# Kernel tuning notes

Measured on AMD Instinct MI355X. Metric: run time of the kernel, lower is better.

## Reference

```python
import jax, jax.numpy as jnp
import numpy as np

ENERGY = 0.4  # target low-frequency energy ratio (ctor default energy=0.4)


def setup_inputs() -> dict:
    key = jax.random.key(0)
    x = jax.random.normal(key, (8, 64, 256, 256), dtype=jnp.float32)
    return {"x": x}


def _min_cutoff_map(H, W):
    """For each pixel of the fftshifted spectrum, the smallest cutoff c such that
    the pixel lies inside the central box [crow-c:crow+c, ccol-c:ccol+c].
    A pixel (r, cc) is inside iff c >= max(-dr, dr+1) and c >= max(-dc, dc+1)."""
    crow, ccol = H // 2, W // 2
    dr = np.arange(H) - crow
    dc = np.arange(W) - ccol
    mr = np.maximum(-dr, dr + 1)
    mc = np.maximum(-dc, dc + 1)
    return np.maximum(mr[:, None], mc[None, :]).astype(np.int32)  # [H, W]


def reference(x):
    B, C, H, W = x.shape
    # fp32 FFT (matches the autocast-disabled fft in the original)
    fshift = jnp.fft.fftshift(jnp.fft.fft2(x.astype(jnp.float32)), axes=(-2, -1))

    minc = jnp.asarray(_min_cutoff_map(H, W))          # [H, W] int32
    nseg = max(H // 2, W // 2) + 1                      # static
    K = min(H, W) // 2                                  # candidates are 1..K-1

    # Radial (box) cumulative energy profile of channel 0, one pass per sample.
    mag2 = jnp.abs(fshift[:, 0]) ** 2                   # [B, H, W]
    ids = minc.reshape(-1)
    per_box = jax.vmap(
        lambda m: jax.ops.segment_sum(m.reshape(-1), ids, num_segments=nseg)
    )(mag2)                                             # [B, nseg]
    cum = jnp.cumsum(per_box, axis=-1)                  # cum[b, c] = box-energy at cutoff c
    total = cum[:, -1]
    target = ENERGY * total

    found = cum[:, 1:K] >= target[:, None]              # candidates c = 1..K-1
    first = jnp.argmax(found, axis=-1) + 1              # smallest satisfying c
    cutoff = jnp.where(jnp.any(found, axis=-1), first, 5)  # fallback 5, as in torch

    # Zero the central box per sample (broadcast over channels), then inverse FFT.
    keep = (minc[None, None, :, :] > cutoff[:, None, None, None]).astype(jnp.float32)
    hp = fshift * keep
    out = jnp.abs(jnp.fft.ifft2(jnp.fft.ifftshift(hp, axes=(-2, -1))))
    return out
```

## Files before the change

### kernel.cpp

```cpp
#include <hip/hip_runtime.h>
#include <hip/hip_fp16.h>
#include <math.h>

#define RESERVE 16384

__device__ __forceinline__ float2 cadd(float2 a, float2 b){ return make_float2(a.x+b.x, a.y+b.y); }
__device__ __forceinline__ float2 csub(float2 a, float2 b){ return make_float2(a.x-b.x, a.y-b.y); }
__device__ __forceinline__ float2 cmul(float2 a, float2 b){ return make_float2(a.x*b.x - a.y*b.y, a.x*b.y + a.y*b.x); }
__device__ __forceinline__ float2 cmulc(float2 a, float2 b){
  return make_float2(a.x*b.x + a.y*b.y, a.x*b.y - a.y*b.x); }
__device__ __forceinline__ __half2 f2h(float2 v){ return __floats2half2_rn(v.x, v.y); }
__device__ __forceinline__ float2 h2f(__half2 h){ return __half22float2(h); }

#define SCHED_FENCE() __builtin_amdgcn_sched_barrier(0x7F)

__device__ __forceinline__ constexpr int rho4(int r) { return ((r & 3) << 2) | (r >> 2); }

template<int DIR> __device__ __forceinline__ float2 twc(float2 z, float c, float s) {
  const float si = (DIR < 0) ? s : -s;
  return make_float2(c*z.x - si*z.y, c*z.y + si*z.x);
}
template<int DIR> __device__ __forceinline__ float2 mulmi(float2 z) {
  return (DIR < 0) ? make_float2(z.y, -z.x) : make_float2(-z.y, z.x);
}

template<int DIR, bool REV>
__device__ __forceinline__ void fft16(float2* v) {
  #define IX(i) (REV ? rho4(i) : (i))
  #pragma unroll
  for (int j0 = 0; j0 < 4; ++j0) {
    float2 a0 = v[IX(j0)], a1 = v[IX(j0+4)], a2 = v[IX(j0+8)], a3 = v[IX(j0+12)];
    float2 t0 = cadd(a0,a2), t1 = csub(a0,a2), t2 = cadd(a1,a3), d = csub(a1,a3);
    float2 t3 = (DIR < 0) ? make_float2(d.y,-d.x) : make_float2(-d.y,d.x);
    v[IX(j0)]    = cadd(t0,t2);
    v[IX(j0+4)]  = cadd(t1,t3);
    v[IX(j0+8)]  = csub(t0,t2);
    v[IX(j0+12)] = csub(t1,t3);
  }
  v[IX(5)]  = twc<DIR>(v[IX(5)],  0.92387953f, -0.38268343f);
  v[IX(6)]  = twc<DIR>(v[IX(6)],  0.70710678f, -0.70710678f);
  v[IX(7)]  = twc<DIR>(v[IX(7)],  0.38268343f, -0.92387953f);
  v[IX(9)]  = twc<DIR>(v[IX(9)],  0.70710678f, -0.70710678f);
  v[IX(10)] = mulmi<DIR>(v[IX(10)]);
  v[IX(11)] = twc<DIR>(v[IX(11)], -0.70710678f, -0.70710678f);
  v[IX(13)] = twc<DIR>(v[IX(13)],  0.38268343f, -0.92387953f);
  v[IX(14)] = twc<DIR>(v[IX(14)], -0.70710678f, -0.70710678f);
  v[IX(15)] = twc<DIR>(v[IX(15)], -0.92387953f,  0.38268343f);
  #pragma unroll
  for (int k1 = 0; k1 < 4; ++k1) {
    float2 a0 = v[IX(4*k1)], a1 = v[IX(4*k1+1)], a2 = v[IX(4*k1+2)], a3 = v[IX(4*k1+3)];
    float2 t0 = cadd(a0,a2), t1 = csub(a0,a2), t2 = cadd(a1,a3), d = csub(a1,a3);
    float2 t3 = (DIR < 0) ? make_float2(d.y,-d.x) : make_float2(-d.y,d.x);
    v[IX(4*k1)]   = cadd(t0,t2);
    v[IX(4*k1+1)] = cadd(t1,t3);
    v[IX(4*k1+2)] = csub(t0,t2);
    v[IX(4*k1+3)] = csub(t1,t3);
  }
  #undef IX
}

__device__ __forceinline__ void make_twf(int l, float2* twf) {
  float s, c;
  sincospif((float)l * (-1.0f/128.0f), &s, &c);
  const float2 w = make_float2(c, s);
  twf[0] = make_float2(1.f, 0.f);
  #pragma unroll
  for (int k = 1; k < 16; ++k) twf[k] = cmul(twf[k-1], w);
}

template<int DIR, bool REV1, bool HB>
__device__ __forceinline__ void fft256g(float2* v, void* trb, int l, const float2* twf) {
  fft16<DIR, REV1>(v);
  #pragma unroll
  for (int r = 0; r < 16; ++r) {
    const int k1 = REV1 ? r : rho4(r);
    float2 z = v[r];
    z = (DIR < 0) ? cmul(twf[k1], z) : cmulc(twf[k1], z);
    const int idx = (k1 << 4) | (l ^ k1);
    if (HB) ((__half2*)trb)[idx] = f2h(z);
    else    ((float2*)trb)[idx] = z;
  }
  SCHED_FENCE();
  #pragma unroll
  for (int j = 0; j < 16; ++j) {
    const int idx = (l << 4) | (j ^ l);
    v[j] = HB ? h2f(((__half2*)trb)[idx]) : ((float2*)trb)[idx];
  }
  SCHED_FENCE();
  fft16<DIR, false>(v);
}

__global__ __launch_bounds__(256) void k_pass1(const float* __restrict__ x,
    __half2* __restrict__ Bt, int img0, int istep) {
  __shared__ __align__(16) char smraw[16 * 264 * 8];
  float2*  trb  = (float2*)smraw;
  __half2* tile = (__half2*)smraw;
  const int tid = threadIdx.x, g = tid >> 4, l = tid & 15;
  const int slot = blockIdx.y, img = img0 + slot * istep;
  float2 twf[16]; make_twf(l, twf);
  const float* xim = x + ((size_t)img << 16);
  __half2* bim = Bt + ((size_t)slot << 16);
  float2* tb = trb + g * 264;
  #pragma unroll 1
  for (int it = 0; it < 4; ++it) {
    const int row = (blockIdx.x << 6) + (it << 4) + g;
    const float* xr = xim + (row << 8);
    float2 v[16];
    #pragma unroll
    for (int j = 0; j < 16; ++j) v[j] = make_float2(xr[l + (j << 4)], 0.f);
    fft256g<-1, false, false>(v, tb, l, twf);
    __syncthreads();
    #pragma unroll
    for (int rr = 0; rr < 16; ++rr)
      tile[(l + (rho4(rr) << 4)) * 17 + g] = f2h(v[rr]);
    __syncthreads();
    const int rbase = (blockIdx.x << 6) + (it << 4);
    const int rloc = tid & 15, ub = tid >> 4;
    #pragma unroll
    for (int jj = 0; jj < 16; ++jj) {
      const int u = (jj << 4) + ub;
      bim[(u << 8) + rbase + rloc] = tile[u * 17 + rloc];
    }
    __syncthreads();
  }
}

__global__ __launch_bounds__(256) void k_pass2(const __half2* __restrict__ Bt,
    __half2* __restrict__ Ct, const int* __restrict__ cutoffs, int img0, int istep) {
  __shared__ __align__(16) char smraw[256 * 17 * 4];
  __half2* trb  = (__half2*)smraw;
  __half2* tile = (__half2*)smraw;
  const int tid = threadIdx.x, g = tid >> 4, l = tid & 15;
  const int slot = blockIdx.y, img = img0 + slot * istep;
  const int cut = cutoffs[img >> 6];
  float2 twf[16]; make_twf(l, twf);
  const __half2* bim = Bt + ((size_t)slot << 16);
  __half2* cim = Ct + ((size_t)slot << 16);
  __half2* tb = trb + g * 264;
  #pragma unroll 1
  for (int it = 0; it < 4; ++it) {
    const int u = (blockIdx.x << 6) + (it << 4) + g;
    const __half2* col = bim + (u << 8);
    float2 v[16];
    #pragma unroll
    for (int j = 0; j < 16; ++j) v[j] = h2f(col[l + (j << 4)]);
    fft256g<-1, false, true>(v, tb, l, twf);
    if ((u < cut) | (u >= 256 - cut)) {
      #pragma unroll
      for (int rr = 0; rr < 16; ++rr) {
        const int vi = l + (rho4(rr) << 4);
        if (vi < cut || vi >= 256 - cut) v[rr] = make_float2(0.f, 0.f);
      }
    }
    fft256g<1, true, true>(v, tb, l, twf);
    __syncthreads();
    #pragma unroll
    for (int rr = 0; rr < 16; ++rr)
      tile[(l + (rho4(rr) << 4)) * 17 + g] = f2h(v[rr]);
    __syncthreads();
    const int ubase = (blockIdx.x << 6) + (it << 4);
    const int cloc = tid & 15, rb = tid >> 4;
    #pragma unroll
    for (int jj = 0; jj < 16; ++jj) {
      const int r = (jj << 4) + rb;
      cim[(r << 8) + ubase + cloc] = tile[r * 17 + cloc];
    }
    __syncthreads();
  }
}

__global__ __launch_bounds__(256) void k_pass3(const __half2* __restrict__ Ct,
    float* __restrict__ out, int img0, int istep) {
  __shared__ __half2 trbs[16 * 264];
  const int tid = threadIdx.x, g = tid >> 4, l = tid & 15;
  const int slot = blockIdx.y, img = img0 + slot * istep;
  float2 twf[16]; make_twf(l, twf);
  #pragma unroll
  for (int k = 0; k < 16; ++k) { twf[k].x *= 0.0625f; twf[k].y *= 0.0625f; }
  const __half2* cim = Ct + ((size_t)slot << 16);
  float* oim = out + ((size_t)img << 16);
  __half2* tb = trbs + g * 264;
  #pragma unroll 1
  for (int it = 0; it < 4; ++it) {
    const int row = (blockIdx.x << 6) + (it << 4) + g;
    const __half2* rp = cim + (row << 8);
    float2 v[16];
    #pragma unroll
    for (int j = 0; j < 16; ++j) v[j] = h2f(rp[l + (j << 4)]);
    fft256g<1, false, true>(v, tb, l, twf);
    float* orow = oim + (row << 8);
    #pragma unroll
    for (int rr = 0; rr < 16; ++rr) {
      const float2 z = v[rr];
      orow[l + (rho4(rr) << 4)] = sqrtf(z.x*z.x + z.y*z.y) * (1.f/4096.f);
    }
  }
}

__global__ __launch_bounds__(256) void k_hist(const __half2* __restrict__ Bt,
    double* __restrict__ bins, int slot0, int sstep, int batch0) {
  __shared__ float2 trbuf[16 * 256];
  __shared__ float whist[4][132];
  const int tid = threadIdx.x, g = tid >> 4, l = tid & 15, wave = tid >> 6;
  const int lb = blockIdx.y;
  const int batch = batch0 + lb;
  const size_t slot = (size_t)(slot0 + lb * sstep);
  const int u = (blockIdx.x << 4) + g;
  float2 twf[16]; make_twf(l, twf);
  for (int i = tid & 63; i < 132; i += 64) whist[wave][i] = 0.f;
  __syncthreads();
  const __half2* col = Bt + (slot << 16) + (u << 8);
  float2 v[16];
  #pragma unroll
  for (int j = 0; j < 16; ++j) v[j] = h2f(col[l + (j << 4)]);
  float2* tb = trbuf + (g << 8);
  fft256g<-1, false, false>(v, tb, l, twf);
  const int fc = (u < 128) ? u + 1 : 256 - u;
  #pragma unroll
  for (int rr = 0; rr < 16; ++rr) {
    const int vi = l + (rho4(rr) << 4);
    const int fu = (vi < 128) ? vi + 1 : 256 - vi;
    const int seg = fu > fc ? fu : fc;
    const float2 z = v[rr];
    atomicAdd(&whist[wave][seg], z.x*z.x + z.y*z.y);
  }
  __syncthreads();
  for (int s = tid; s < 129; s += 256) {
    const float sum = whist[0][s] + whist[1][s] + whist[2][s] + whist[3][s];
    if (sum != 0.f) atomicAdd(&bins[batch * 129 + s], (double)sum);
  }
}

__global__ void k_cutoff(const double* __restrict__ bins, int* __restrict__ cutoffs) {
  const int b = threadIdx.x;
  if (b < 8) {
    const double* Bv = bins + b * 129;
    double total = 0.0;
    for (int s = 0; s < 129; ++s) total += Bv[s];
    const double target = 0.4 * total;
    double cum = Bv[0];
    int cut = 5;
    bool found = false;
    for (int s = 1; s <= 127; ++s) {
      cum += Bv[s];
      if (!found && cum >= target) { cut = s; found = true; }
    }
    cutoffs[b] = cut;
  }
}

extern "C" void kernel_launch(void* const* d_in, const int* in_sizes, int n_in,
                              void* d_out, int out_size, void* d_ws, size_t ws_size,
                              hipStream_t stream) {
  const float* x = (const float*)d_in[0];
  float* out = (float*)d_out;
  char* wsb = (char*)d_ws;
  double* bins    = (double*)wsb;
  int*    cutoffs = (int*)(wsb + 8448);
  char*   payload = wsb + RESERVE;

  size_t avail = (ws_size > RESERVE) ? ws_size - (size_t)RESERVE : 0;
  long long Gl = (long long)(avail / 524288);
  int G = (Gl > 512) ? 512 : (int)Gl;
  if (G < 1) G = 1;
  __half2* Bt = (__half2*)payload;
  __half2* Ct = (__half2*)(payload + (size_t)G * 262144);

  hipMemsetAsync(bins, 0, 8 * 129 * sizeof(double), stream);
  dim3 blk(256, 1, 1);

  if (G >= 512) {
    k_pass1<<<dim3(4, 512), blk, 0, stream>>>(x, Bt, 0, 1);
    k_hist <<<dim3(16, 8),  blk, 0, stream>>>(Bt, bins, 0, 64, 0);
    k_cutoff<<<dim3(1), dim3(64), 0, stream>>>(bins, cutoffs);
    k_pass2<<<dim3(4, 512), blk, 0, stream>>>(Bt, Ct, cutoffs, 0, 1);
    k_pass3<<<dim3(4, 512), blk, 0, stream>>>(Ct, out, 0, 1);
  } else {
    int Gp = G > 8 ? 8 : G;
    for (int b0 = 0; b0 < 8; b0 += Gp) {
      int n = (8 - b0 < Gp) ? (8 - b0) : Gp;
      k_pass1<<<dim3(4, n), blk, 0, stream>>>(x, Bt, b0 * 64, 64);
      k_hist <<<dim3(16, n), blk, 0, stream>>>(Bt, bins, 0, 1, b0);
    }
    k_cutoff<<<dim3(1), dim3(64), 0, stream>>>(bins, cutoffs);
    for (int g0 = 0; g0 < 512; g0 += G) {
      int n = (512 - g0 < G) ? (512 - g0) : G;
      k_pass1<<<dim3(4, n), blk, 0, stream>>>(x, Bt, g0, 1);
      k_pass2<<<dim3(4, n), blk, 0, stream>>>(Bt, Ct, cutoffs, g0, 1);
      k_pass3<<<dim3(4, n), blk, 0, stream>>>(Ct, out, g0, 1);
    }
  }
}
```

Measured before the change: 254.6 us.

## Split pass1/pass2 into one tile per block and pad shared transpose buffers

Pass1 and pass2 now handle one 16-row/column tile per block instead of looping over four, so their grids grow fourfold. Global loads are issued before twiddle setup to hide latency. The in-register FFT transpose changes from an XOR-swizzled layout to a padded stride-17 layout, with the per-group buffer stride widened. Pass3 also uses a raw hardware sqrt. The aim is more parallelism and latency hiding, at the cost of more blocks and repeated twiddle setup.

```diff
diff --git a/kernel.cpp b/kernel.cpp
--- a/kernel.cpp
+++ b/kernel.cpp
@@ -71,107 +71,112 @@
 template<int DIR, bool REV1, bool HB>
 __device__ __forceinline__ void fft256g(float2* v, void* trb, int l, const float2* twf) {
   fft16<DIR, REV1>(v);
-  #pragma unroll
-  for (int r = 0; r < 16; ++r) {
-    const int k1 = REV1 ? r : rho4(r);
-    float2 z = v[r];
-    z = (DIR < 0) ? cmul(twf[k1], z) : cmulc(twf[k1], z);
-    const int idx = (k1 << 4) | (l ^ k1);
-    if (HB) ((__half2*)trb)[idx] = f2h(z);
-    else    ((float2*)trb)[idx] = z;
-  }
-  SCHED_FENCE();
-  #pragma unroll
-  for (int j = 0; j < 16; ++j) {
-    const int idx = (l << 4) | (j ^ l);
-    v[j] = HB ? h2f(((__half2*)trb)[idx]) : ((float2*)trb)[idx];
+  if (HB) {
+    __half2* t = (__half2*)trb;
+    #pragma unroll
+    for (int r = 0; r < 16; ++r) {
+      const int k1 = REV1 ? r : rho4(r);
+      float2 z = v[r];
+      z = (DIR < 0) ? cmul(twf[k1], z) : cmulc(twf[k1], z);
+      t[k1 * 17 + l] = f2h(z);
+    }
+    SCHED_FENCE();
+    #pragma unroll
+    for (int j = 0; j < 16; ++j) v[j] = h2f(t[l * 17 + j]);
+  } else {
+    float2* t = (float2*)trb;
+    #pragma unroll
+    for (int r = 0; r < 16; ++r) {
+      const int k1 = REV1 ? r : rho4(r);
+      float2 z = v[r];
+      z = (DIR < 0) ? cmul(twf[k1], z) : cmulc(twf[k1], z);
+      t[k1 * 17 + l] = z;
+    }
+    SCHED_FENCE();
+    #pragma unroll
+    for (int j = 0; j < 16; ++j) v[j] = ((float2*)trb)[l * 17 + j];
   }
   SCHED_FENCE();
   fft16<DIR, false>(v);
 }
 
+#define GS32 276
+#define GS16 280
+
 __global__ __launch_bounds__(256) void k_pass1(const float* __restrict__ x,
     __half2* __restrict__ Bt, int img0, int istep) {
-  __shared__ __align__(16) char smraw[16 * 264 * 8];
+  __shared__ __align__(16) char smraw[16 * GS32 * 8];
   float2*  trb  = (float2*)smraw;
   __half2* tile = (__half2*)smraw;
   const int tid = threadIdx.x, g = tid >> 4, l = tid & 15;
   const int slot = blockIdx.y, img = img0 + slot * istep;
-  float2 twf[16]; make_twf(l, twf);
-  const float* xim = x + ((size_t)img << 16);
-  __half2* bim = Bt + ((size_t)slot << 16);
-  float2* tb = trb + g * 264;
-  #pragma unroll 1
-  for (int it = 0; it < 4; ++it) {
-    const int row = (blockIdx.x << 6) + (it << 4) + g;
-    const float* xr = xim + (row << 8);
-    float2 v[16];
-    #pragma unroll
-    for (int j = 0; j < 16; ++j) v[j] = make_float2(xr[l + (j << 4)], 0.f);
-    fft256g<-1, false, false>(v, tb, l, twf);
-    __syncthreads();
-    #pragma unroll
-    for (int rr = 0; rr < 16; ++rr)
-      tile[(l + (rho4(rr) << 4)) * 17 + g] = f2h(v[rr]);
-    __syncthreads();
-    const int rbase = (blockIdx.x << 6) + (it << 4);
-    const int rloc = tid & 15, ub = tid >> 4;
-    #pragma unroll
-    for (int jj = 0; jj < 16; ++jj) {
-      const int u = (jj << 4) + ub;
-      bim[(u << 8) + rbase + rloc] = tile[u * 17 + rloc];
-    }
-    __syncthreads();
+  const int row = (blockIdx.x << 4) + g;
+  const float* xr = x + ((size_t)img << 16) + (row << 8);
+  float rv[16];
+  #pragma unroll
+  for (int j = 0; j < 16; ++j) rv[j] = xr[l + (j << 4)];
+  float2 twf[16]; make_twf(l, twf);
+  float2 v[16];
+  #pragma unroll
+  for (int j = 0; j < 16; ++j) v[j] = make_float2(rv[j], 0.f);
+  fft256g<-1, false, false>(v, trb + g * GS32, l, twf);
+  __syncthreads();
+  #pragma unroll
+  for (int rr = 0; rr < 16; ++rr)
+    tile[(l + (rho4(rr) << 4)) * 17 + g] = f2h(v[rr]);
+  __syncthreads();
+  __half2* bo = Bt + ((size_t)slot << 16) + (blockIdx.x << 4);
+  const int rloc = tid & 15, ub = tid >> 4;
+  #pragma unroll
+  for (int jj = 0; jj < 16; ++jj) {
+    const int u = (jj << 4) + ub;
+    bo[(u << 8) + rloc] = tile[u * 17 + rloc];
   }
 }
 
 __global__ __launch_bounds__(256) void k_pass2(const __half2* __restrict__ Bt,
     __half2* __restrict__ Ct, const int* __restrict__ cutoffs, int img0, int istep) {
-  __shared__ __align__(16) char smraw[256 * 17 * 4];
+  __shared__ __align__(16) char smraw[16 * GS16 * 4];
   __half2* trb  = (__half2*)smraw;
   __half2* tile = (__half2*)smraw;
   const int tid = threadIdx.x, g = tid >> 4, l = tid & 15;
   const int slot = blockIdx.y, img = img0 + slot * istep;
+  const int u = (blockIdx.x << 4) + g;
+  const __half2* col = Bt + ((size_t)slot << 16) + (u << 8);
+  __half2 hv[16];
+  #pragma unroll
+  for (int j = 0; j < 16; ++j) hv[j] = col[l + (j << 4)];
   const int cut = cutoffs[img >> 6];
   float2 twf[16]; make_twf(l, twf);
-  const __half2* bim = Bt + ((size_t)slot << 16);
-  __half2* cim = Ct + ((size_t)slot << 16);
-  __half2* tb = trb + g * 264;
-  #pragma unroll 1
-  for (int it = 0; it < 4; ++it) {
-    const int u = (blockIdx.x << 6) + (it << 4) + g;
-    const __half2* col = bim + (u << 8);
-    float2 v[16];
-    #pragma unroll
-    for (int j = 0; j < 16; ++j) v[j] = h2f(col[l + (j << 4)]);
-    fft256g<-1, false, true>(v, tb, l, twf);
-    if ((u < cut) | (u >= 256 - cut)) {
-      #pragma unroll
-      for (int rr = 0; rr < 16; ++rr) {
-        const int vi = l + (rho4(rr) << 4);
-        if (vi < cut || vi >= 256 - cut) v[rr] = make_float2(0.f, 0.f);
-      }
-    }
-    fft256g<1, true, true>(v, tb, l, twf);
-    __syncthreads();
-    #pragma unroll
-    for (int rr = 0; rr < 16; ++rr)
-      tile[(l + (rho4(rr) << 4)) * 17 + g] = f2h(v[rr]);
-    __syncthreads();
-    const int ubase = (blockIdx.x << 6) + (it << 4);
-    const int cloc = tid & 15, rb = tid >> 4;
-    #pragma unroll
-    for (int jj = 0; jj < 16; ++jj) {
-      const int r = (jj << 4) + rb;
-      cim[(r << 8) + ubase + cloc] = tile[r * 17 + cloc];
-    }
-    __syncthreads();
+  float2 v[16];
+  #pragma unroll
+  for (int j = 0; j < 16; ++j) v[j] = h2f(hv[j]);
+  fft256g<-1, false, true>(v, trb + g * GS16, l, twf);
+  if ((u < cut) | (u >= 256 - cut)) {
+    #pragma unroll
+    for (int rr = 0; rr < 16; ++rr) {
+      const int vi = l + (rho4(rr) << 4);
+      if (vi < cut || vi >= 256 - cut) v[rr] = make_float2(0.f, 0.f);
+    }
+  }
+  fft256g<1, true, true>(v, trb + g * GS16, l, twf);
+  __syncthreads();
+  #pragma unroll
+  for (int rr = 0; rr < 16; ++rr)
+    tile[(l + (rho4(rr) << 4)) * 17 + g] = f2h(v[rr]);
+  __syncthreads();
+  __half2* co = Ct + ((size_t)slot << 16) + (blockIdx.x << 4);
+  const int cloc = tid & 15, rb = tid >> 4;
+  #pragma unroll
+  for (int jj = 0; jj < 16; ++jj) {
+    const int r = (jj << 4) + rb;
+    co[(r << 8) + cloc] = tile[r * 17 + cloc];
   }
 }
 
 __global__ __launch_bounds__(256) void k_pass3(const __half2* __restrict__ Ct,
     float* __restrict__ out, int img0, int istep) {
-  __shared__ __half2 trbs[16 * 264];
+  __shared__ __half2 trbs[16 * GS16];
   const int tid = threadIdx.x, g = tid >> 4, l = tid & 15;
   const int slot = blockIdx.y, img = img0 + slot * istep;
   float2 twf[16]; make_twf(l, twf);
@@ -179,7 +184,7 @@
   for (int k = 0; k < 16; ++k) { twf[k].x *= 0.0625f; twf[k].y *= 0.0625f; }
   const __half2* cim = Ct + ((size_t)slot << 16);
   float* oim = out + ((size_t)img << 16);
-  __half2* tb = trbs + g * 264;
+  __half2* tb = trbs + g * GS16;
   #pragma unroll 1
   for (int it = 0; it < 4; ++it) {
     const int row = (blockIdx.x << 6) + (it << 4) + g;
@@ -192,14 +197,14 @@
     #pragma unroll
     for (int rr = 0; rr < 16; ++rr) {
       const float2 z = v[rr];
-      orow[l + (rho4(rr) << 4)] = sqrtf(z.x*z.x + z.y*z.y) * (1.f/4096.f);
+      orow[l + (rho4(rr) << 4)] = __builtin_amdgcn_sqrtf(z.x*z.x + z.y*z.y) * (1.f/4096.f);
     }
   }
 }
 
 __global__ __launch_bounds__(256) void k_hist(const __half2* __restrict__ Bt,
     double* __restrict__ bins, int slot0, int sstep, int batch0) {
-  __shared__ float2 trbuf[16 * 256];
+  __shared__ float2 trbuf[16 * GS32];
   __shared__ float whist[4][132];
   const int tid = threadIdx.x, g = tid >> 4, l = tid & 15, wave = tid >> 6;
   const int lb = blockIdx.y;
@@ -213,8 +218,7 @@
   float2 v[16];
   #pragma unroll
   for (int j = 0; j < 16; ++j) v[j] = h2f(col[l + (j << 4)]);
-  float2* tb = trbuf + (g << 8);
-  fft256g<-1, false, false>(v, tb, l, twf);
+  fft256g<-1, false, false>(v, trbuf + g * GS32, l, twf);
   const int fc = (u < 128) ? u + 1 : 256 - u;
   #pragma unroll
   for (int rr = 0; rr < 16; ++rr) {
@@ -270,24 +274,24 @@
   dim3 blk(256, 1, 1);
 
   if (G >= 512) {
-    k_pass1<<<dim3(4, 512), blk, 0, stream>>>(x, Bt, 0, 1);
-    k_hist <<<dim3(16, 8),  blk, 0, stream>>>(Bt, bins, 0, 64, 0);
+    k_pass1<<<dim3(16, 512), blk, 0, stream>>>(x, Bt, 0, 1);
+    k_hist <<<dim3(16, 8),   blk, 0, stream>>>(Bt, bins, 0, 64, 0);
     k_cutoff<<<dim3(1), dim3(64), 0, stream>>>(bins, cutoffs);
-    k_pass2<<<dim3(4, 512), blk, 0, stream>>>(Bt, Ct, cutoffs, 0, 1);
-    k_pass3<<<dim3(4, 512), blk, 0, stream>>>(Ct, out, 0, 1);
+    k_pass2<<<dim3(16, 512), blk, 0, stream>>>(Bt, Ct, cutoffs, 0, 1);
+    k_pass3<<<dim3(4, 512),  blk, 0, stream>>>(Ct, out, 0, 1);
   } else {
     int Gp = G > 8 ? 8 : G;
     for (int b0 = 0; b0 < 8; b0 += Gp) {
       int n = (8 - b0 < Gp) ? (8 - b0) : Gp;
-      k_pass1<<<dim3(4, n), blk, 0, stream>>>(x, Bt, b0 * 64, 64);
+      k_pass1<<<dim3(16, n), blk, 0, stream>>>(x, Bt, b0 * 64, 64);
       k_hist <<<dim3(16, n), blk, 0, stream>>>(Bt, bins, 0, 1, b0);
     }
     k_cutoff<<<dim3(1), dim3(64), 0, stream>>>(bins, cutoffs);
     for (int g0 = 0; g0 < 512; g0 += G) {
       int n = (512 - g0 < G) ? (512 - g0) : G;
-      k_pass1<<<dim3(4, n), blk, 0, stream>>>(x, Bt, g0, 1);
-      k_pass2<<<dim3(4, n), blk, 0, stream>>>(Bt, Ct, cutoffs, g0, 1);
-      k_pass3<<<dim3(4, n), blk, 0, stream>>>(Ct, out, g0, 1);
-    }
-  }
-}
+      k_pass1<<<dim3(16, n), blk, 0, stream>>>(x, Bt, g0, 1);
+      k_pass2<<<dim3(16, n), blk, 0, stream>>>(Bt, Ct, cutoffs, g0, 1);
+      k_pass3<<<dim3(4, n),  blk, 0, stream>>>(Ct, out, g0, 1);
+    }
+  }
+}
```

Result: faster. 227.2 us (-10.7%).
